# Kernel tuning notes

Measured on AMD Instinct MI355X. Metric: run time of the kernel, lower is better.

The kernel has to match this reference:

```python
import jax, jax.numpy as jnp
import numpy as np

D_MODEL = 768
D_FF = 3072
N_HEADS = 12
D_QUART = D_MODEL // 4  # 192
EPS = 1e-5


def layer_norm(x, g, b):
    mu = jnp.mean(x, axis=-1, keepdims=True)
    var = jnp.mean((x - mu) ** 2, axis=-1, keepdims=True)
    return (x - mu) * jax.lax.rsqrt(var + EPS) * g + b


def setup_inputs() -> dict:
    key = jax.random.key(0)
    ks = jax.random.split(key, 24)
    d, dff, dq = D_MODEL, D_FF, D_QUART
    s = lambda k, shape, fan: jax.random.normal(k, shape, jnp.float32) * (1.0 / np.sqrt(fan))
    return {
        "x": jax.random.normal(ks[0], (8, 1024, d), jnp.float32),
        # distance_proj: Linear(1, d//4) -> weight [dq], bias [dq]
        "dp_w": s(ks[1], (dq,), 1), "dp_b": jnp.zeros((dq,), jnp.float32),
        # spatial_encoding: Linear(d,d) GELU Linear(d,d)
        "se_w1": s(ks[2], (d, d), d), "se_b1": jnp.zeros((d,), jnp.float32),
        "se_w2": s(ks[3], (d, d), d), "se_b2": jnp.zeros((d,), jnp.float32),
        # attention projections (stored [in, out])
        "wq": s(ks[4], (d, d), d), "bq": jnp.zeros((d,), jnp.float32),
        "wk": s(ks[5], (d, d), d), "bk": jnp.zeros((d,), jnp.float32),
        "wv": s(ks[6], (d, d), d), "bv": jnp.zeros((d,), jnp.float32),
        "wo": s(ks[7], (d, d), d), "bo": jnp.zeros((d,), jnp.float32),
        # geometric_net FFN
        "gw1": s(ks[8], (d, dff), d), "gb1": jnp.zeros((dff,), jnp.float32),
        "gw2": s(ks[9], (dff, d), dff), "gb2": jnp.zeros((d,), jnp.float32),
        # layer norms
        "n1_g": jnp.ones((d,), jnp.float32), "n1_b": jnp.zeros((d,), jnp.float32),
        "n2_g": jnp.ones((d,), jnp.float32), "n2_b": jnp.zeros((d,), jnp.float32),
    }


def _forward(x, dp_w, dp_b, se_w1, se_b1, se_w2, se_b2,
             wq, bq, wk, bk, wv, bv, wo, bo,
             gw1, gb1, gw2, gb2, n1_g, n1_b, n2_g, n2_b):
    B, N, d = x.shape
    # --- compute_spatial_features ---
    # ||x_i - x_j|| via Gram trick (avoids [B,N,N,d] intermediate)
    sq = jnp.sum(x * x, axis=-1)                      # [B,N]
    gram = jnp.einsum('bnd,bmd->bnm', x, x)           # [B,N,N]
    d2 = jnp.maximum(sq[:, :, None] + sq[:, None, :] - 2.0 * gram, 0.0)
    dist = jnp.sqrt(d2)                               # [B,N,N]
    # Linear(1, d/4) then mean over j commutes: project the mean distance
    mean_d = jnp.mean(dist, axis=2)                   # [B,N]
    spat = mean_d[..., None] * dp_w + dp_b            # [B,N,d/4]
    spat = jnp.pad(spat, ((0, 0), (0, 0), (0, d - D_QUART)))  # [B,N,d]
    # spatial_encoding MLP (exact GELU, matching torch nn.GELU default)
    h = jax.nn.gelu(spat @ se_w1 + se_b1, approximate=False)
    x = x + (h @ se_w2 + se_b2)
    # --- attention block ---
    res = x
    xn = layer_norm(x, n1_g, n1_b)
    H, dh = N_HEADS, d // N_HEADS
    q = (xn @ wq + bq).reshape(B, N, H, dh)
    k = (xn @ wk + bk).reshape(B, N, H, dh)
    v = (xn @ wv + bv).reshape(B, N, H, dh)
    scores = jnp.einsum('bqhd,bkhd->bhqk', q, k) / np.sqrt(dh)
    attn = jax.nn.softmax(scores, axis=-1)
    o = jnp.einsum('bhqk,bkhd->bqhd', attn, v).reshape(B, N, d)
    x = res + (o @ wo + bo)
    # --- FFN block ---
    res = x
    xn = layer_norm(x, n2_g, n2_b)
    h = jax.nn.gelu(xn @ gw1 + gb1, approximate=False)
    x = res + (h @ gw2 + gb2)
    return x


def reference(x, dp_w, dp_b, se_w1, se_b1, se_w2, se_b2,
              wq, bq, wk, bk, wv, bv, wo, bo,
              gw1, gb1, gw2, gb2, n1_g, n1_b, n2_g, n2_b):
    return _forward(x, dp_w, dp_b, se_w1, se_b1, se_w2, se_b2,
                    wq, bq, wk, bk, wv, bv, wo, bo,
                    gw1, gb1, gw2, gb2, n1_g, n1_b, n2_g, n2_b)
```

## Files before the change

### kernel.cpp

```cpp
#include <hip/hip_runtime.h>
#include <hip/hip_bf16.h>

typedef unsigned short ushort;
typedef __attribute__((ext_vector_type(8))) __bf16 bf16x8;
typedef __attribute__((ext_vector_type(4))) float f32x4;
typedef __attribute__((ext_vector_type(8))) ushort ushort8;

__device__ inline ushort f2bf(float f) {
    union { float f; unsigned u; } a{f};
    unsigned r = a.u + 0x7FFFu + ((a.u >> 16) & 1u);
    return (ushort)(r >> 16);
}
__device__ inline float gelu_f(float x) {
    return 0.5f * x * (1.f + erff(x * 0.70710678118654752f));
}

__global__ void transpose_to_bf16(const float* __restrict__ Wm, ushort* __restrict__ Wt, int K, int N) {
    __shared__ float tile[32][33];
    int k0 = blockIdx.x * 32, n0 = blockIdx.y * 32;
    int tx = threadIdx.x, ty = threadIdx.y;
    #pragma unroll
    for (int r = ty; r < 32; r += 8) tile[r][tx] = Wm[(size_t)(k0 + r) * N + n0 + tx];
    __syncthreads();
    #pragma unroll
    for (int r = ty; r < 32; r += 8) Wt[(size_t)(n0 + r) * K + k0 + tx] = f2bf(tile[tx][r]);
}

__global__ void rowstat(const float* __restrict__ x, ushort* __restrict__ xb, float* __restrict__ sq) {
    int row = blockIdx.x;
    const float* xr = x + (size_t)row * 768;
    ushort* xbr = xb + (size_t)row * 768;
    int t = threadIdx.x;
    float s = 0.f;
    #pragma unroll
    for (int i = 0; i < 3; ++i) {
        float vv = xr[t + i * 256];
        xbr[t + i * 256] = f2bf(vv);
        s += vv * vv;
    }
    #pragma unroll
    for (int off = 1; off < 64; off <<= 1) s += __shfl_xor(s, off);
    __shared__ float wsum[4];
    if ((t & 63) == 0) wsum[t >> 6] = s;
    __syncthreads();
    if (t == 0) sq[row] = wsum[0] + wsum[1] + wsum[2] + wsum[3];
}

__global__ void precomp_ac(const float* __restrict__ dp_w, const float* __restrict__ dp_b,
                           const float* __restrict__ se_w1, const float* __restrict__ se_b1,
                           float* __restrict__ Avec, float* __restrict__ Cvec) {
    int o = blockIdx.x * 256 + threadIdx.x;
    float a = 0.f, c = 0.f;
    for (int i = 0; i < 192; ++i) {
        float w = se_w1[(size_t)i * 768 + o];
        a += dp_w[i] * w;
        c += dp_b[i] * w;
    }
    Avec[o] = a;
    Cvec[o] = c + se_b1[o];
}

__global__ void hgen(const float* __restrict__ mean_acc, const float* __restrict__ Avec,
                     const float* __restrict__ Cvec, ushort* __restrict__ h) {
    int row = blockIdx.x;
    float md = mean_acc[row] * (1.f / 1024.f);
    int t = threadIdx.x;
    #pragma unroll
    for (int i = 0; i < 3; ++i) {
        int o = t + i * 256;
        h[(size_t)row * 768 + o] = f2bf(gelu_f(md * Avec[o] + Cvec[o]));
    }
}

__global__ void lnorm(const float* __restrict__ xin, const float* __restrict__ g,
                      const float* __restrict__ b, ushort* __restrict__ xn) {
    int row = blockIdx.x;
    const float* xr = xin + (size_t)row * 768;
    int t = threadIdx.x;
    float v[3];
    float s = 0.f, s2 = 0.f;
    #pragma unroll
    for (int i = 0; i < 3; ++i) {
        v[i] = xr[t + i * 256];
        s += v[i];
        s2 += v[i] * v[i];
    }
    #pragma unroll
    for (int off = 1; off < 64; off <<= 1) { s += __shfl_xor(s, off); s2 += __shfl_xor(s2, off); }
    __shared__ float a0[4], a1[4];
    if ((t & 63) == 0) { a0[t >> 6] = s; a1[t >> 6] = s2; }
    __syncthreads();
    s = a0[0] + a0[1] + a0[2] + a0[3];
    s2 = a1[0] + a1[1] + a1[2] + a1[3];
    float mu = s * (1.f / 768.f);
    float var = s2 * (1.f / 768.f) - mu * mu;
    float rs = rsqrtf(var + 1e-5f);
    #pragma unroll
    for (int i = 0; i < 3; ++i) {
        int o = t + i * 256;
        xn[(size_t)row * 768 + o] = f2bf((v[i] - mu) * rs * g[o] + b[o]);
    }
}

#define BM 128
#define BK 32

enum { EPI_BF16 = 0, EPI_GELU = 1, EPI_RES = 2, EPI_GRAM = 3, EPI_QKV = 4 };

template <int EPI, int BNT>
__launch_bounds__(256, BNT == 64 ? 4 : 2)
__global__ void gemm_bt(const ushort* __restrict__ A, const ushort* __restrict__ Bt,
                        int M, int N, int K,
                        const float* __restrict__ bias,
                        const float* res, float* outf,
                        ushort* __restrict__ outh,
                        const float* __restrict__ sq, float* __restrict__ mean_acc) {
    __shared__ __align__(16) ushort As[2][BM * BK];
    __shared__ __align__(16) ushort Bs[2][BNT * BK];

    unsigned gx = gridDim.x, gy = gridDim.y;
    unsigned flat = blockIdx.x + gx * (blockIdx.y + gy * blockIdx.z);
    unsigned total = gx * gy * gridDim.z;
    unsigned chunk = total >> 3;
    flat = (flat & 7) * chunk + (flat >> 3);
    unsigned bx = flat % gx;
    unsigned rem = flat / gx;
    unsigned by = rem % gy;
    unsigned bz = rem / gy;

    int m0 = bx * BM;
    int n0 = by * BNT;
    if (EPI == EPI_GRAM) {
        A += (size_t)bz * 1024 * 768;
        Bt = A;
        sq += bz * 1024;
        mean_acc += bz * 1024;
    }
    int t = threadIdx.x, w = t >> 6, l = t & 63;
    int lg = l >> 4, li = l & 15;
    constexpr int MI = (BNT == 128) ? 4 : 2;
    int wm = (BNT == 128) ? (w >> 1) * 64 : w * 32;
    int wn = (BNT == 128) ? (w & 1) * 64 : 0;

    int srow = l >> 2, scol = (l & 3) * 8;
    const ushort* agp0 = A + (size_t)(m0 + (2 * w) * 16 + srow) * K + scol;
    const ushort* agp1 = A + (size_t)(m0 + (2 * w + 1) * 16 + srow) * K + scol;
    const ushort* bgp0;
    const ushort* bgp1 = nullptr;
    ushort* la0 = &As[0][(2 * w) * 16 * BK];
    ushort* lb0;
    if (BNT == 128) {
        bgp0 = Bt + (size_t)(n0 + (2 * w) * 16 + srow) * K + scol;
        bgp1 = Bt + (size_t)(n0 + (2 * w + 1) * 16 + srow) * K + scol;
        lb0 = &Bs[0][(2 * w) * 16 * BK];
    } else {
        bgp0 = Bt + (size_t)(n0 + w * 16 + srow) * K + scol;
        lb0 = &Bs[0][w * 16 * BK];
    }

    f32x4 acc[MI][4] = {};

    auto stage = [&](int buf, int kt) {
        size_t ko = (size_t)kt * BK;
        ushort* la = la0 + buf * (BM * BK);
        ushort* lb = lb0 + buf * (BNT * BK);
        __builtin_amdgcn_global_load_lds((const __attribute__((address_space(1))) void*)(agp0 + ko),
                                         (__attribute__((address_space(3))) void*)la, 16, 0, 0);
        __builtin_amdgcn_global_load_lds((const __attribute__((address_space(1))) void*)(agp1 + ko),
                                         (__attribute__((address_space(3))) void*)(la + 16 * BK), 16, 0, 0);
        __builtin_amdgcn_global_load_lds((const __attribute__((address_space(1))) void*)(bgp0 + ko),
                                         (__attribute__((address_space(3))) void*)lb, 16, 0, 0);
        if (BNT == 128)
            __builtin_amdgcn_global_load_lds((const __attribute__((address_space(1))) void*)(bgp1 + ko),
                                             (__attribute__((address_space(3))) void*)(lb + 16 * BK), 16, 0, 0);
    };

    int nk = K / BK;
    stage(0, 0);
    __syncthreads();
    int buf = 0;
    for (int kt = 0; kt < nk; ++kt) {
        if (kt + 1 < nk) stage(buf ^ 1, kt + 1);
        bf16x8 af[MI], bfr[4];
        #pragma unroll
        for (int i = 0; i < MI; ++i)
            af[i] = *reinterpret_cast<const bf16x8*>(&As[buf][(wm + i * 16 + li) * BK + lg * 8]);
        #pragma unroll
        for (int i = 0; i < 4; ++i)
            bfr[i] = *reinterpret_cast<const bf16x8*>(&Bs[buf][(wn + i * 16 + li) * BK + lg * 8]);
        #pragma unroll
        for (int mi = 0; mi < MI; ++mi)
            #pragma unroll
            for (int ni = 0; ni < 4; ++ni)
                acc[mi][ni] = __builtin_amdgcn_mfma_f32_16x16x32_bf16(af[mi], bfr[ni], acc[mi][ni], 0, 0, 0);
        __syncthreads();
        buf ^= 1;
    }

    #pragma unroll
    for (int mi = 0; mi < MI; ++mi) {
        #pragma unroll
        for (int r = 0; r < 4; ++r) {
            int row = m0 + wm + mi * 16 + lg * 4 + r;
            if (EPI == EPI_GRAM) {
                float si = sq[row];
                float s = 0.f;
                #pragma unroll
                for (int ni = 0; ni < 4; ++ni) {
                    int col = n0 + wn + ni * 16 + li;
                    float d2 = si + sq[col] - 2.f * acc[mi][ni][r];
                    s += sqrtf(fmaxf(d2, 0.f));
                }
                s += __shfl_xor(s, 1); s += __shfl_xor(s, 2);
                s += __shfl_xor(s, 4); s += __shfl_xor(s, 8);
                if (li == 0) atomicAdd(&mean_acc[row], s);
            } else {
                #pragma unroll
                for (int ni = 0; ni < 4; ++ni) {
                    int col = n0 + wn + ni * 16 + li;
                    float v = acc[mi][ni][r] + bias[col];
                    if (EPI == EPI_BF16) outh[(size_t)row * N + col] = f2bf(v);
                    if (EPI == EPI_GELU) outh[(size_t)row * N + col] = f2bf(gelu_f(v));
                    if (EPI == EPI_RES) outf[(size_t)row * N + col] = res[(size_t)row * N + col] + v;
                    if (EPI == EPI_QKV) {
                        int which = col / 768;
                        int c2 = col - which * 768;
                        outh[(size_t)which * (8192 * 768) + (size_t)row * 768 + c2] = f2bf(v);
                    }
                }
            }
        }
    }
}

__launch_bounds__(256, 3)
__global__ void flash_attn(const ushort* __restrict__ q, const ushort* __restrict__ k,
                           const ushort* __restrict__ v, ushort* __restrict__ o) {
    int flat = blockIdx.x + 8 * (blockIdx.y + 12 * blockIdx.z);
    flat = (flat & 7) * 96 + (flat >> 3);
    int qt = flat & 7;
    int rem = flat >> 3;
    int h = rem % 12;
    int b = rem / 12;

    int t = threadIdx.x, w = t >> 6, l = t & 63;
    int lg = l >> 4, li = l & 15;

    __shared__ __align__(16) ushort Vt[2][64][72];
    __shared__ __align__(16) ushort P[4][32][72];

    const size_t hoff = (size_t)h * 64;
    const size_t bbase = (size_t)b * 1024 * 768;

    bf16x8 qf[2][2];
    #pragma unroll
    for (int f = 0; f < 2; ++f) {
        int qrow = qt * 128 + w * 32 + f * 16 + li;
        const ushort* qp = &q[bbase + (size_t)qrow * 768 + hoff];
        qf[f][0] = *reinterpret_cast<const bf16x8*>(qp + lg * 8);
        qf[f][1] = *reinterpret_cast<const bf16x8*>(qp + 32 + lg * 8);
    }

    float m_[2][4], ell[2][4];
    f32x4 oacc[2][4];
    #pragma unroll
    for (int f = 0; f < 2; ++f)
        #pragma unroll
        for (int r = 0; r < 4; ++r) { m_[f][r] = -1e30f; ell[f][r] = 0.f; }
    #pragma unroll
    for (int f = 0; f < 2; ++f)
        #pragma unroll
        for (int n = 0; n < 4; ++n) oacc[f][n] = f32x4{0.f, 0.f, 0.f, 0.f};

    int vrow = t & 63;
    int vc = t >> 6;
    const ushort* vbase = &v[bbase + hoff];

    ushort8 vv0 = *reinterpret_cast<const ushort8*>(&vbase[(size_t)vrow * 768 + vc * 8]);
    ushort8 vv1 = *reinterpret_cast<const ushort8*>(&vbase[(size_t)vrow * 768 + (vc + 4) * 8]);

    for (int jt = 0; jt < 16; ++jt) {
        int j0 = jt * 64, buf = jt & 1;
        #pragma unroll
        for (int i = 0; i < 8; ++i) Vt[buf][vc * 8 + i][vrow] = vv0[i];
        #pragma unroll
        for (int i = 0; i < 8; ++i) Vt[buf][(vc + 4) * 8 + i][vrow] = vv1[i];
        if (jt < 15) {
            vv0 = *reinterpret_cast<const ushort8*>(&vbase[(size_t)(j0 + 64 + vrow) * 768 + vc * 8]);
            vv1 = *reinterpret_cast<const ushort8*>(&vbase[(size_t)(j0 + 64 + vrow) * 768 + (vc + 4) * 8]);
        }
        bf16x8 kf0[4], kf1[4];
        #pragma unroll
        for (int jj = 0; jj < 4; ++jj) {
            const ushort* kp = &k[bbase + (size_t)(j0 + jj * 16 + li) * 768 + hoff];
            kf0[jj] = *reinterpret_cast<const bf16x8*>(kp + lg * 8);
            kf1[jj] = *reinterpret_cast<const bf16x8*>(kp + 32 + lg * 8);
        }
        f32x4 s[2][4];
        #pragma unroll
        for (int jj = 0; jj < 4; ++jj)
            #pragma unroll
            for (int f = 0; f < 2; ++f) {
                f32x4 a = {0.f, 0.f, 0.f, 0.f};
                a = __builtin_amdgcn_mfma_f32_16x16x32_bf16(qf[f][0], kf0[jj], a, 0, 0, 0);
                a = __builtin_amdgcn_mfma_f32_16x16x32_bf16(qf[f][1], kf1[jj], a, 0, 0, 0);
                s[f][jj] = a * 0.125f;
            }
        #pragma unroll
        for (int f = 0; f < 2; ++f) {
            float mt[4];
            #pragma unroll
            for (int r = 0; r < 4; ++r)
                mt[r] = fmaxf(fmaxf(s[f][0][r], s[f][1][r]), fmaxf(s[f][2][r], s[f][3][r]));
            #pragma unroll
            for (int r = 0; r < 4; ++r) {
                mt[r] = fmaxf(mt[r], __shfl_xor(mt[r], 1));
                mt[r] = fmaxf(mt[r], __shfl_xor(mt[r], 2));
                mt[r] = fmaxf(mt[r], __shfl_xor(mt[r], 4));
                mt[r] = fmaxf(mt[r], __shfl_xor(mt[r], 8));
            }
            float al[4], ps[4];
            #pragma unroll
            for (int r = 0; r < 4; ++r) {
                float mn = fmaxf(m_[f][r], mt[r]);
                al[r] = __expf(m_[f][r] - mn);
                m_[f][r] = mn;
                float p0 = __expf(s[f][0][r] - mn);
                float p1 = __expf(s[f][1][r] - mn);
                float p2 = __expf(s[f][2][r] - mn);
                float p3 = __expf(s[f][3][r] - mn);
                s[f][0][r] = p0; s[f][1][r] = p1; s[f][2][r] = p2; s[f][3][r] = p3;
                ps[r] = (p0 + p1) + (p2 + p3);
            }
            #pragma unroll
            for (int r = 0; r < 4; ++r) {
                ps[r] += __shfl_xor(ps[r], 1); ps[r] += __shfl_xor(ps[r], 2);
                ps[r] += __shfl_xor(ps[r], 4); ps[r] += __shfl_xor(ps[r], 8);
                ell[f][r] = ell[f][r] * al[r] + ps[r];
            }
            #pragma unroll
            for (int n = 0; n < 4; ++n)
                #pragma unroll
                for (int r = 0; r < 4; ++r) oacc[f][n][r] *= al[r];
            #pragma unroll
            for (int jj = 0; jj < 4; ++jj)
                #pragma unroll
                for (int r = 0; r < 4; ++r)
                    P[w][f * 16 + lg * 4 + r][jj * 16 + li] = f2bf(s[f][jj][r]);
        }
        __syncthreads();
        bf16x8 pf[2][2];
        #pragma unroll
        for (int f = 0; f < 2; ++f) {
            pf[f][0] = *reinterpret_cast<const bf16x8*>(&P[w][f * 16 + li][lg * 8]);
            pf[f][1] = *reinterpret_cast<const bf16x8*>(&P[w][f * 16 + li][32 + lg * 8]);
        }
        #pragma unroll
        for (int n = 0; n < 4; ++n) {
            bf16x8 vf0 = *reinterpret_cast<const bf16x8*>(&Vt[buf][n * 16 + li][lg * 8]);
            bf16x8 vf1 = *reinterpret_cast<const bf16x8*>(&Vt[buf][n * 16 + li][32 + lg * 8]);
            #pragma unroll
            for (int f = 0; f < 2; ++f) {
                oacc[f][n] = __builtin_amdgcn_mfma_f32_16x16x32_bf16(pf[f][0], vf0, oacc[f][n], 0, 0, 0);
                oacc[f][n] = __builtin_amdgcn_mfma_f32_16x16x32_bf16(pf[f][1], vf1, oacc[f][n], 0, 0, 0);
            }
        }
    }
    #pragma unroll
    for (int f = 0; f < 2; ++f)
        #pragma unroll
        for (int n = 0; n < 4; ++n)
            #pragma unroll
            for (int r = 0; r < 4; ++r) {
                int row = qt * 128 + w * 32 + f * 16 + lg * 4 + r;
                o[bbase + (size_t)row * 768 + hoff + n * 16 + li] = f2bf(oacc[f][n][r] / ell[f][r]);
            }
}

extern "C" void kernel_launch(void* const* d_in, const int* in_sizes, int n_in,
                              void* d_out, int out_size, void* d_ws, size_t ws_size,
                              hipStream_t stream) {
    const float* x = (const float*)d_in[0];
    const float* dp_w = (const float*)d_in[1];
    const float* dp_b = (const float*)d_in[2];
    const float* se_w1 = (const float*)d_in[3];
    const float* se_b1 = (const float*)d_in[4];
    const float* se_w2 = (const float*)d_in[5];
    const float* se_b2 = (const float*)d_in[6];
    const float* wq = (const float*)d_in[7];  const float* bq = (const float*)d_in[8];
    const float* wk = (const float*)d_in[9];  const float* bk = (const float*)d_in[10];
    const float* wv = (const float*)d_in[11]; const float* bv = (const float*)d_in[12];
    const float* wo = (const float*)d_in[13]; const float* bo = (const float*)d_in[14];
    const float* gw1 = (const float*)d_in[15]; const float* gb1 = (const float*)d_in[16];
    const float* gw2 = (const float*)d_in[17]; const float* gb2 = (const float*)d_in[18];
    const float* n1g = (const float*)d_in[19]; const float* n1b = (const float*)d_in[20];
    const float* n2g = (const float*)d_in[21]; const float* n2b = (const float*)d_in[22];
    float* out = (float*)d_out;

    constexpr size_t SZ_ACT = (size_t)8192 * 768 * 2;
    char* W = (char*)d_ws;
    ushort* xb = (ushort*)(W);
    ushort* q_ = (ushort*)(W + SZ_ACT);
    ushort* k_ = (ushort*)(W + 2 * SZ_ACT);
    ushort* v_ = (ushort*)(W + 3 * SZ_ACT);
    ushort* o_ = (ushort*)(W + 4 * SZ_ACT);
    ushort* hsp = q_;
    ushort* hff = q_;
    ushort* wqt = (ushort*)(W + 5 * SZ_ACT);
    ushort* wkt = wqt + (size_t)768 * 768;
    ushort* wvt = wkt + (size_t)768 * 768;
    ushort* wot = wvt + (size_t)768 * 768;
    ushort* sw2t = wot + (size_t)768 * 768;
    ushort* g1t = sw2t + (size_t)768 * 768;
    ushort* g2t = g1t + (size_t)768 * 3072;
    float* sqv = (float*)(g2t + (size_t)3072 * 768);
    float* meanv = sqv + 8192;
    float* Avec = meanv + 8192;
    float* Cvec = Avec + 768;
    float* bqkv = Cvec + 768;

    dim3 tb(32, 8);
    transpose_to_bf16<<<dim3(24, 24), tb, 0, stream>>>(se_w2, sw2t, 768, 768);
    transpose_to_bf16<<<dim3(24, 24), tb, 0, stream>>>(wq, wqt, 768, 768);
    transpose_to_bf16<<<dim3(24, 24), tb, 0, stream>>>(wk, wkt, 768, 768);
    transpose_to_bf16<<<dim3(24, 24), tb, 0, stream>>>(wv, wvt, 768, 768);
    transpose_to_bf16<<<dim3(24, 24), tb, 0, stream>>>(wo, wot, 768, 768);
    transpose_to_bf16<<<dim3(24, 96), tb, 0, stream>>>(gw1, g1t, 768, 3072);
    transpose_to_bf16<<<dim3(96, 24), tb, 0, stream>>>(gw2, g2t, 3072, 768);
    hipMemcpyAsync(bqkv, bq, 768 * sizeof(float), hipMemcpyDeviceToDevice, stream);
    hipMemcpyAsync(bqkv + 768, bk, 768 * sizeof(float), hipMemcpyDeviceToDevice, stream);
    hipMemcpyAsync(bqkv + 1536, bv, 768 * sizeof(float), hipMemcpyDeviceToDevice, stream);

    rowstat<<<8192, 256, 0, stream>>>(x, xb, sqv);
    precomp_ac<<<3, 256, 0, stream>>>(dp_w, dp_b, se_w1, se_b1, Avec, Cvec);
    hipMemsetAsync(meanv, 0, 8192 * sizeof(float), stream);

    gemm_bt<EPI_GRAM, 128><<<dim3(8, 8, 8), 256, 0, stream>>>(xb, xb, 1024, 1024, 768,
                                                              nullptr, nullptr, nullptr, nullptr, sqv, meanv);
    hgen<<<8192, 256, 0, stream>>>(meanv, Avec, Cvec, hsp);
    gemm_bt<EPI_RES, 64><<<dim3(64, 12), 256, 0, stream>>>(hsp, sw2t, 8192, 768, 768,
                                                           se_b2, x, out, nullptr, nullptr, nullptr);
    lnorm<<<8192, 256, 0, stream>>>(out, n1g, n1b, xb);
    gemm_bt<EPI_QKV, 128><<<dim3(64, 18), 256, 0, stream>>>(xb, wqt, 8192, 2304, 768,
                                                            bqkv, nullptr, nullptr, q_, nullptr, nullptr);
    flash_attn<<<dim3(8, 12, 8), 256, 0, stream>>>(q_, k_, v_, o_);
    gemm_bt<EPI_RES, 64><<<dim3(64, 12), 256, 0, stream>>>(o_, wot, 8192, 768, 768,
                                                           bo, out, out, nullptr, nullptr, nullptr);
    lnorm<<<8192, 256, 0, stream>>>(out, n2g, n2b, xb);
    gemm_bt<EPI_GELU, 128><<<dim3(64, 24), 256, 0, stream>>>(xb, g1t, 8192, 3072, 768,
                                                             gb1, nullptr, nullptr, hff, nullptr, nullptr);
    gemm_bt<EPI_RES, 64><<<dim3(64, 12), 256, 0, stream>>>(hff, g2t, 8192, 768, 3072,
                                                           gb2, out, out, nullptr, nullptr, nullptr);
}
```

Before: 469.5 us.

## Add 256x128-tile 8-wave GEMM with triple-buffered direct-to-LDS loads for big GEMMs

Introduces a new GEMM kernel with 512 threads and a 256x128 output tile, a 3-stage pipeline of global_load_lds async copies, and XOR-swizzled LDS layout. It replaces the QKV, FFN-up (GELU) and FFN-down (residual) GEMMs. The aim is higher arithmetic intensity per block and better latency hiding of global loads. The trade-off is larger LDS use (about 144KB per block) and fewer blocks (e.g. 192 for the FFN-down GEMM), which may underfill the CUs.

Result: slower. 502.1 us (+7.0%).

```diff
diff --git a/kernel.cpp b/kernel.cpp
--- a/kernel.cpp
+++ b/kernel.cpp
@@ -233,6 +233,115 @@
     }
 }
 
+template <int EPI>
+__launch_bounds__(512, 2)
+__global__ void gemm8(const ushort* __restrict__ A, const ushort* __restrict__ Bt,
+                      int M, int N, int K,
+                      const float* __restrict__ bias,
+                      const float* res, float* outf, ushort* __restrict__ outh) {
+    __shared__ __align__(16) ushort As[3][2][128 * 64];
+    __shared__ __align__(16) ushort Bs[3][2][64 * 64];
+
+    unsigned gx = gridDim.x, gy = gridDim.y;
+    unsigned flat = blockIdx.x + gx * blockIdx.y;
+    unsigned total = gx * gy;
+    unsigned chunk = total >> 3;
+    flat = (flat & 7) * chunk + (flat >> 3);
+    int m0 = (flat % gx) * 256;
+    int n0 = (flat / gx) * 128;
+
+    int t = threadIdx.x, w = t >> 6, l = t & 63;
+    int lg = l >> 4, li = l & 15;
+    int wr = w >> 1, wc = w & 1;
+    int ha = wr >> 1;
+    int ra = (wr & 1) * 64;
+
+    f32x4 acc[4][4] = {};
+
+    auto stage = [&](int buf, int kt) {
+        int k0 = kt * 64;
+        #pragma unroll
+        for (int h = 0; h < 2; ++h) {
+            #pragma unroll
+            for (int jj = 0; jj < 2; ++jj) {
+                int d = (2 * w + jj) * 1024 + l * 16;
+                int dp = d ^ (((d >> 9) & 3) << 5);
+                const ushort* src = A + (size_t)(m0 + h * 128 + (dp >> 7)) * K + k0 + ((dp & 127) >> 1);
+                __builtin_amdgcn_global_load_lds(
+                    (const __attribute__((address_space(1))) void*)src,
+                    (__attribute__((address_space(3))) void*)&As[buf][h][(2 * w + jj) * 512], 16, 0, 0);
+            }
+            {
+                int d = w * 1024 + l * 16;
+                int dp = d ^ (((d >> 9) & 3) << 5);
+                const ushort* src = Bt + (size_t)(n0 + h * 64 + (dp >> 7)) * K + k0 + ((dp & 127) >> 1);
+                __builtin_amdgcn_global_load_lds(
+                    (const __attribute__((address_space(1))) void*)src,
+                    (__attribute__((address_space(3))) void*)&Bs[buf][h][w * 512], 16, 0, 0);
+            }
+        }
+    };
+
+    int nk = K / 64;
+    stage(0, 0);
+    stage(1, 1);
+    stage(2, 2);
+    for (int kt = 0; kt < nk; ++kt) {
+        int buf = kt % 3;
+        if (kt + 2 < nk)      asm volatile("s_waitcnt vmcnt(12)" ::: "memory");
+        else if (kt + 1 < nk) asm volatile("s_waitcnt vmcnt(6)" ::: "memory");
+        else                  asm volatile("s_waitcnt vmcnt(0)" ::: "memory");
+        asm volatile("s_barrier" ::: "memory");
+        __builtin_amdgcn_sched_barrier(0);
+        #pragma unroll
+        for (int kk = 0; kk < 2; ++kk) {
+            bf16x8 af[4], bf[4];
+            #pragma unroll
+            for (int mi = 0; mi < 4; ++mi) {
+                int e = (ra + mi * 16 + li) * 128 + kk * 64 + lg * 16;
+                int ep = e ^ (((e >> 9) & 3) << 5);
+                af[mi] = *reinterpret_cast<const bf16x8*>(&As[buf][ha][ep >> 1]);
+            }
+            #pragma unroll
+            for (int ni = 0; ni < 4; ++ni) {
+                int e = (ni * 16 + li) * 128 + kk * 64 + lg * 16;
+                int ep = e ^ (((e >> 9) & 3) << 5);
+                bf[ni] = *reinterpret_cast<const bf16x8*>(&Bs[buf][wc][ep >> 1]);
+            }
+            __builtin_amdgcn_s_setprio(1);
+            #pragma unroll
+            for (int mi = 0; mi < 4; ++mi)
+                #pragma unroll
+                for (int ni = 0; ni < 4; ++ni)
+                    acc[mi][ni] = __builtin_amdgcn_mfma_f32_16x16x32_bf16(af[mi], bf[ni], acc[mi][ni], 0, 0, 0);
+            __builtin_amdgcn_s_setprio(0);
+        }
+        asm volatile("s_barrier" ::: "memory");
+        __builtin_amdgcn_sched_barrier(0);
+        if (kt + 3 < nk) stage(buf, kt + 3);
+    }
+
+    #pragma unroll
+    for (int mi = 0; mi < 4; ++mi) {
+        #pragma unroll
+        for (int r = 0; r < 4; ++r) {
+            int row = m0 + wr * 64 + mi * 16 + lg * 4 + r;
+            #pragma unroll
+            for (int ni = 0; ni < 4; ++ni) {
+                int col = n0 + wc * 64 + ni * 16 + li;
+                float v = acc[mi][ni][r] + bias[col];
+                if (EPI == EPI_GELU) outh[(size_t)row * N + col] = f2bf(gelu_f(v));
+                if (EPI == EPI_RES)  outf[(size_t)row * N + col] = res[(size_t)row * N + col] + v;
+                if (EPI == EPI_QKV) {
+                    int which = col / 768;
+                    int c2 = col - which * 768;
+                    outh[(size_t)which * (8192 * 768) + (size_t)row * 768 + c2] = f2bf(v);
+                }
+            }
+        }
+    }
+}
+
 __launch_bounds__(256, 3)
 __global__ void flash_attn(const ushort* __restrict__ q, const ushort* __restrict__ k,
                            const ushort* __restrict__ v, ushort* __restrict__ o) {
@@ -441,14 +550,14 @@
     gemm_bt<EPI_RES, 64><<<dim3(64, 12), 256, 0, stream>>>(hsp, sw2t, 8192, 768, 768,
                                                            se_b2, x, out, nullptr, nullptr, nullptr);
     lnorm<<<8192, 256, 0, stream>>>(out, n1g, n1b, xb);
-    gemm_bt<EPI_QKV, 128><<<dim3(64, 18), 256, 0, stream>>>(xb, wqt, 8192, 2304, 768,
-                                                            bqkv, nullptr, nullptr, q_, nullptr, nullptr);
+    gemm8<EPI_QKV><<<dim3(32, 18), 512, 0, stream>>>(xb, wqt, 8192, 2304, 768,
+                                                     bqkv, nullptr, nullptr, q_);
     flash_attn<<<dim3(8, 12, 8), 256, 0, stream>>>(q_, k_, v_, o_);
     gemm_bt<EPI_RES, 64><<<dim3(64, 12), 256, 0, stream>>>(o_, wot, 8192, 768, 768,
                                                            bo, out, out, nullptr, nullptr, nullptr);
     lnorm<<<8192, 256, 0, stream>>>(out, n2g, n2b, xb);
-    gemm_bt<EPI_GELU, 128><<<dim3(64, 24), 256, 0, stream>>>(xb, g1t, 8192, 3072, 768,
-                                                             gb1, nullptr, nullptr, hff, nullptr, nullptr);
-    gemm_bt<EPI_RES, 64><<<dim3(64, 12), 256, 0, stream>>>(hff, g2t, 8192, 768, 3072,
-                                                           gb2, out, out, nullptr, nullptr, nullptr);
-}
+    gemm8<EPI_GELU><<<dim3(32, 24), 512, 0, stream>>>(xb, g1t, 8192, 3072, 768,
+                                                      gb1, nullptr, nullptr, hff);
+    gemm8<EPI_RES><<<dim3(32, 6), 512, 0, stream>>>(hff, g2t, 8192, 768, 3072,
+                                                    gb2, out, out, nullptr);
+}
```
